# Optimization experiments

Measured on AMD Instinct MI355X. Metric: run time of the kernel, lower is better.

## Reference

```python
import jax, jax.numpy as jnp
import numpy as np

EMBED_DIM = 1024
NUM_HEADS = 16
HEAD_DIM = EMBED_DIM // NUM_HEADS
SCALE = float(np.sqrt(HEAD_DIM))


def setup_inputs() -> dict:
    key = jax.random.key(0)
    ks = jax.random.split(key, 7)
    B, S, E = 2, 2048, EMBED_DIM
    query = jax.random.normal(ks[0], (B, S, E), dtype=jnp.float32)
    key_t = jax.random.normal(ks[1], (B, S, E), dtype=jnp.float32)
    value = jax.random.normal(ks[2], (B, S, E), dtype=jnp.float32)
    # nn.Linear(E, E, bias=False): weight shape (out, in); y = x @ W.T
    std = 1.0 / np.sqrt(E)
    Wq = jax.random.uniform(ks[3], (E, E), jnp.float32, -std, std)
    Wk = jax.random.uniform(ks[4], (E, E), jnp.float32, -std, std)
    Wv = jax.random.uniform(ks[5], (E, E), jnp.float32, -std, std)
    Wo = jax.random.uniform(ks[6], (E, E), jnp.float32, -std, std)
    return {"query": query, "key": key_t, "value": value,
            "Wq": Wq, "Wk": Wk, "Wv": Wv, "Wo": Wo}


def reference(query, key, value, Wq, Wk, Wv, Wo):
    B, S, E = query.shape
    H, D = NUM_HEADS, HEAD_DIM
    q = (query @ Wq.T).reshape(B, S, H, D).transpose(0, 2, 1, 3)  # [B,H,S,D]
    k = (key @ Wk.T).reshape(B, S, H, D).transpose(0, 2, 1, 3)
    v = (value @ Wv.T).reshape(B, S, H, D).transpose(0, 2, 1, 3)
    scores = jnp.einsum('bhqd,bhkd->bhqk', q, k) / SCALE  # [B,H,S,S]
    attn = jax.nn.softmax(scores, axis=-1)
    out = jnp.einsum('bhqk,bhkd->bhqd', attn, v)  # [B,H,S,D]
    out = out.transpose(0, 2, 1, 3).reshape(B, S, E)
    return out @ Wo.T
```

## Files before the change

### kernel.cpp

```cpp
#include <hip/hip_runtime.h>
#include <hip/hip_bf16.h>
#include <math.h>

typedef float f32x4 __attribute__((ext_vector_type(4)));
typedef __bf16 bf16x8 __attribute__((ext_vector_type(8)));
typedef unsigned short u16;
typedef u16 u16x8 __attribute__((ext_vector_type(8)));
typedef u16 u16x4 __attribute__((ext_vector_type(4)));

__device__ __forceinline__ u16 f2bf(float f) {
    unsigned u = __builtin_bit_cast(unsigned, f);
    u = (u + 0x7fffu + ((u >> 16) & 1u)) >> 16;
    return (u16)u;
}
__device__ __forceinline__ unsigned pack2_rhu(float a, float b) {
    return __builtin_amdgcn_perm(__builtin_bit_cast(unsigned, b) + 0x8000u,
                                 __builtin_bit_cast(unsigned, a) + 0x8000u,
                                 0x07060302u);
}

#if __has_builtin(__builtin_amdgcn_exp2f)
#define EXP2(x) __builtin_amdgcn_exp2f(x)
#else
#define EXP2(x) exp2f(x)
#endif

__device__ __forceinline__ void gload16(const u16* g, u16* l) {
    __builtin_amdgcn_global_load_lds(
        (const __attribute__((address_space(1))) unsigned int*)(g),
        (__attribute__((address_space(3))) unsigned int*)(l), 16, 0, 0);
}

__global__ __launch_bounds__(256) void cast_all(
    const float* __restrict__ q, const float* __restrict__ k, const float* __restrict__ v,
    const float* __restrict__ wq, const float* __restrict__ wk, const float* __restrict__ wv,
    const float* __restrict__ wo, u16* __restrict__ dst) {
    int i = blockIdx.x * 256 + threadIdx.x;
    const float* src;
    int off;
    if (i < 3145728) {
        int seg = i >> 20;
        src = (seg == 0) ? q : (seg == 1) ? k : v;
        off = i - (seg << 20);
    } else {
        int j = (i - 3145728) >> 18;
        src = (j == 0) ? wq : (j == 1) ? wk : (j == 2) ? wv : wo;
        off = (i - 3145728) - (j << 18);
    }
    float4 val = ((const float4*)src)[off];
    u16x4 o4;
    o4.x = f2bf(val.x); o4.y = f2bf(val.y); o4.z = f2bf(val.z); o4.w = f2bf(val.w);
    ((u16x4*)dst)[i] = o4;
}

__global__ __launch_bounds__(256) void qkv_gemm(
    const u16* __restrict__ Xq, const u16* __restrict__ Xk, const u16* __restrict__ Xv,
    const u16* __restrict__ Wq, const u16* __restrict__ Wk, const u16* __restrict__ Wv,
    u16* __restrict__ Qo, u16* __restrict__ Ko, u16* __restrict__ Vto) {
    constexpr int K = 1024;
    const int z = blockIdx.z;
    const u16* __restrict__ A = (z == 0) ? Xq : (z == 1) ? Xk : Xv;
    const u16* __restrict__ W = (z == 0) ? Wq : (z == 1) ? Wk : Wv;
    u16* __restrict__ Out = (z == 0) ? Qo : (z == 1) ? Ko : Vto;

    __shared__ __align__(16) u16 As[128 * 64];
    __shared__ __align__(16) u16 Bs[128 * 64];

    const int t = threadIdx.x;
    const int lane = t & 63, wave = t >> 6;
    const int quad = lane >> 4, c = lane & 15, cx = c & 7;
    const int wr = (wave >> 1) * 64, wc = (wave & 1) * 64;
    const int rowA0 = blockIdx.y * 128;
    const int colB0 = blockIdx.x * 128;

    const int l3 = lane >> 3, l7 = lane & 7;
    const int chs = (l7 ^ l3) << 3;
    const u16* gA[4];
    const u16* gB[4];
    u16* lA[4];
    u16* lB[4];
#pragma unroll
    for (int i = 0; i < 4; ++i) {
        int row = wave * 32 + i * 8 + l3;
        gA[i] = A + (size_t)(rowA0 + row) * K + chs;
        gB[i] = W + (size_t)(colB0 + row) * K + chs;
        lA[i] = As + (wave * 256 + i * 64) * 8;
        lB[i] = Bs + (wave * 256 + i * 64) * 8;
    }

    const f32x4 zero4 = {0.f, 0.f, 0.f, 0.f};
    f32x4 acc[4][4];
#pragma unroll
    for (int i = 0; i < 4; ++i)
#pragma unroll
        for (int j = 0; j < 4; ++j) acc[i][j] = zero4;

    for (int kt = 0; kt < K; kt += 64) {
        __syncthreads();
#pragma unroll
        for (int i = 0; i < 4; ++i) {
            gload16(gA[i] + kt, lA[i]);
            gload16(gB[i] + kt, lB[i]);
        }
        __syncthreads();
#pragma unroll
        for (int ks = 0; ks < 2; ++ks) {
            const int co = ((ks * 4 + quad) ^ cx) << 3;
            bf16x8 af[4], bfr[4];
#pragma unroll
            for (int i = 0; i < 4; ++i)
                af[i] = *(const bf16x8*)(As + (wr + i * 16 + c) * 64 + co);
#pragma unroll
            for (int j = 0; j < 4; ++j)
                bfr[j] = *(const bf16x8*)(Bs + (wc + j * 16 + c) * 64 + co);
            if (z == 2) {
#pragma unroll
                for (int i = 0; i < 4; ++i)
#pragma unroll
                    for (int j = 0; j < 4; ++j)
                        acc[i][j] = __builtin_amdgcn_mfma_f32_16x16x32_bf16(bfr[j], af[i], acc[i][j], 0, 0, 0);
            } else {
#pragma unroll
                for (int i = 0; i < 4; ++i)
#pragma unroll
                    for (int j = 0; j < 4; ++j)
                        acc[i][j] = __builtin_amdgcn_mfma_f32_16x16x32_bf16(af[i], bfr[j], acc[i][j], 0, 0, 0);
            }
        }
    }

    const float scale = (z == 0) ? 0.18033688011112042f : 1.0f;
#pragma unroll
    for (int i = 0; i < 4; ++i) {
#pragma unroll
        for (int j = 0; j < 4; ++j) {
#pragma unroll
            for (int r = 0; r < 4; ++r) {
                float v = acc[i][j][r];
                if (z == 2) {
                    int n = colB0 + wc + j * 16 + quad * 4 + r;
                    int m = rowA0 + wr + i * 16 + c;
                    int b = m >> 11, s = m & 2047, h = n >> 6, d = n & 63;
                    Out[((((b << 4) | h) << 6) + d) * 2048 + s] = f2bf(v);
                } else {
                    int m = rowA0 + wr + i * 16 + quad * 4 + r;
                    int n = colB0 + wc + j * 16 + c;
                    int b = m >> 11, s = m & 2047, h = n >> 6, d = n & 63;
                    Out[((((b << 4) | h) * 2048 + s) << 6) + d] = f2bf(v * scale);
                }
            }
        }
    }
}

__global__ __launch_bounds__(256, 2) void out_gemm(const u16* __restrict__ A,
                                                   const u16* __restrict__ W,
                                                   float* __restrict__ Out) {
    constexpr int K = 1024;
    __shared__ __align__(16) u16 As[64 * 64];
    __shared__ __align__(16) u16 Bs[128 * 64];
    const int t = threadIdx.x;
    const int lane = t & 63, wave = t >> 6;
    const int quad = lane >> 4, c = lane & 15, cx = c & 7;
    const int wr = (wave >> 1) * 32, wc = (wave & 1) * 64;
    const int rowA0 = blockIdx.y * 64;
    const int colB0 = blockIdx.x * 128;

    const int l3 = lane >> 3, l7 = lane & 7;
    const int chs = (l7 ^ l3) << 3;
    const u16* gA[2];
    const u16* gB[4];
    u16* lA[2];
    u16* lB[4];
#pragma unroll
    for (int i = 0; i < 2; ++i) {
        int row = wave * 16 + i * 8 + l3;
        gA[i] = A + (size_t)(rowA0 + row) * K + chs;
        lA[i] = As + (wave * 128 + i * 64) * 8;
    }
#pragma unroll
    for (int i = 0; i < 4; ++i) {
        int row = wave * 32 + i * 8 + l3;
        gB[i] = W + (size_t)(colB0 + row) * K + chs;
        lB[i] = Bs + (wave * 256 + i * 64) * 8;
    }

    const f32x4 zero4 = {0.f, 0.f, 0.f, 0.f};
    f32x4 acc[2][4];
#pragma unroll
    for (int i = 0; i < 2; ++i)
#pragma unroll
        for (int j = 0; j < 4; ++j) acc[i][j] = zero4;

    for (int kt = 0; kt < K; kt += 64) {
        __syncthreads();
#pragma unroll
        for (int i = 0; i < 2; ++i) gload16(gA[i] + kt, lA[i]);
#pragma unroll
        for (int i = 0; i < 4; ++i) gload16(gB[i] + kt, lB[i]);
        __syncthreads();
#pragma unroll
        for (int ks = 0; ks < 2; ++ks) {
            const int co = ((ks * 4 + quad) ^ cx) << 3;
            bf16x8 af[2], bfr[4];
#pragma unroll
            for (int i = 0; i < 2; ++i)
                af[i] = *(const bf16x8*)(As + (wr + i * 16 + c) * 64 + co);
#pragma unroll
            for (int j = 0; j < 4; ++j)
                bfr[j] = *(const bf16x8*)(Bs + (wc + j * 16 + c) * 64 + co);
#pragma unroll
            for (int i = 0; i < 2; ++i)
#pragma unroll
                for (int j = 0; j < 4; ++j)
                    acc[i][j] = __builtin_amdgcn_mfma_f32_16x16x32_bf16(af[i], bfr[j], acc[i][j], 0, 0, 0);
        }
    }
#pragma unroll
    for (int i = 0; i < 2; ++i)
#pragma unroll
        for (int j = 0; j < 4; ++j)
#pragma unroll
            for (int r = 0; r < 4; ++r) {
                int m = rowA0 + wr + i * 16 + quad * 4 + r;
                int n = colB0 + wc + j * 16 + c;
                Out[(m << 10) + n] = acc[i][j][r];
            }
}

__global__ __launch_bounds__(256, 2) void flash_attn(const u16* __restrict__ Qp,
                                                     const u16* __restrict__ Kp,
                                                     const u16* __restrict__ Vt,
                                                     u16* __restrict__ Ob) {
    constexpr int S = 2048;
    const int bh = blockIdx.y;
    const int b = bh >> 4, h = bh & 15;
    const int t = threadIdx.x, wave = t >> 6, lane = t & 63;
    const int quad = lane >> 4, c = lane & 15, cx = c & 7;
    const int qw = blockIdx.x * 128 + wave * 32;
    const u16* Qb = Qp + (bh * S + qw) * 64;
    const u16* Kb = Kp + (bh * S) * 64;
    const u16* Vb = Vt + bh * 64 * S;

    __shared__ __align__(16) u16 Ks[2][64 * 64];
    __shared__ __align__(16) u16 Vs[2][64 * 64];
    __shared__ __align__(16) u16 Ps[4][32 * 64];
    u16* Pw = &Ps[wave][0];

    bf16x8 qf[2][2];
#pragma unroll
    for (int qt = 0; qt < 2; ++qt)
#pragma unroll
        for (int hf = 0; hf < 2; ++hf)
            qf[qt][hf] = *(const bf16x8*)(Qb + (qt * 16 + c) * 64 + hf * 32 + quad * 8);

    const int l3 = lane >> 3, l7 = lane & 7;
    const int chs = (l7 ^ l3) << 3;
    const u16* gK[2];
    const u16* gV[2];
    int lbase[2];
#pragma unroll
    for (int i = 0; i < 2; ++i) {
        int row = wave * 16 + i * 8 + l3;
        gK[i] = Kb + row * 64 + chs;
        gV[i] = Vb + row * 2048 + chs;
        lbase[i] = (wave * 128 + i * 64) * 8;
    }
#pragma unroll
    for (int i = 0; i < 2; ++i) {
        gload16(gK[i], &Ks[0][lbase[i]]);
        gload16(gV[i], &Vs[0][lbase[i]]);
    }
    __syncthreads();

    const f32x4 zero4 = {0.f, 0.f, 0.f, 0.f};
    f32x4 o[2][4];
#pragma unroll
    for (int qt = 0; qt < 2; ++qt)
#pragma unroll
        for (int t2 = 0; t2 < 4; ++t2) o[qt][t2] = zero4;
    float lsum[2] = {0.f, 0.f};

    for (int it = 0; it < S / 64; ++it) {
        const int cur = it & 1;
        if (it + 1 < S / 64) {
#pragma unroll
            for (int i = 0; i < 2; ++i) {
                gload16(gK[i] + (it + 1) * 4096, &Ks[cur ^ 1][lbase[i]]);
                gload16(gV[i] + (it + 1) * 64, &Vs[cur ^ 1][lbase[i]]);
            }
        }
        const u16* Kc = &Ks[cur][0];
        const u16* Vc = &Vs[cur][0];
        const int co0 = (quad ^ cx) << 3, co1 = ((4 + quad) ^ cx) << 3;
        f32x4 sc[4][2];
#pragma unroll
        for (int kt = 0; kt < 4; ++kt) {
            const int krow = (kt * 16 + c) * 64;
            bf16x8 kf0 = *(const bf16x8*)(Kc + krow + co0);
            bf16x8 kf1 = *(const bf16x8*)(Kc + krow + co1);
#pragma unroll
            for (int qt = 0; qt < 2; ++qt) {
                f32x4 zz = zero4;
                zz = __builtin_amdgcn_mfma_f32_16x16x32_bf16(kf0, qf[qt][0], zz, 0, 0, 0);
                zz = __builtin_amdgcn_mfma_f32_16x16x32_bf16(kf1, qf[qt][1], zz, 0, 0, 0);
                sc[kt][qt] = zz;
            }
        }
#pragma unroll
        for (int kt = 0; kt < 4; ++kt) {
            const int pchunk = ((kt * 2 + (quad >> 1)) ^ cx) << 3;
#pragma unroll
            for (int qt = 0; qt < 2; ++qt) {
                float p0 = EXP2(sc[kt][qt][0]);
                float p1 = EXP2(sc[kt][qt][1]);
                float p2 = EXP2(sc[kt][qt][2]);
                float p3 = EXP2(sc[kt][qt][3]);
                lsum[qt] += (p0 + p1) + (p2 + p3);
                uint2 pk;
                pk.x = pack2_rhu(p0, p1);
                pk.y = pack2_rhu(p2, p3);
                *(uint2*)(Pw + (qt * 16 + c) * 64 + pchunk + (quad & 1) * 4) = pk;
            }
        }
        __asm__ __volatile__("s_waitcnt lgkmcnt(0)" ::: "memory");
        bf16x8 pf[2][2];
#pragma unroll
        for (int qt = 0; qt < 2; ++qt) {
            pf[qt][0] = *(const bf16x8*)(Pw + (qt * 16 + c) * 64 + co0);
            pf[qt][1] = *(const bf16x8*)(Pw + (qt * 16 + c) * 64 + co1);
        }
#pragma unroll
        for (int t2 = 0; t2 < 4; ++t2) {
            const int vrow = (t2 * 16 + c) * 64;
            bf16x8 vf0 = *(const bf16x8*)(Vc + vrow + co0);
            bf16x8 vf1 = *(const bf16x8*)(Vc + vrow + co1);
#pragma unroll
            for (int qt = 0; qt < 2; ++qt) {
                o[qt][t2] = __builtin_amdgcn_mfma_f32_16x16x32_bf16(pf[qt][0], vf0, o[qt][t2], 0, 0, 0);
                o[qt][t2] = __builtin_amdgcn_mfma_f32_16x16x32_bf16(pf[qt][1], vf1, o[qt][t2], 0, 0, 0);
            }
        }
        __syncthreads();
    }
#pragma unroll
    for (int qt = 0; qt < 2; ++qt) {
        lsum[qt] += __shfl_xor(lsum[qt], 16);
        lsum[qt] += __shfl_xor(lsum[qt], 32);
    }
#pragma unroll
    for (int qt = 0; qt < 2; ++qt)
#pragma unroll
        for (int r = 0; r < 4; ++r) {
            float inv = 1.f / __shfl(lsum[qt], quad * 4 + r);
            int row = qw + qt * 16 + quad * 4 + r;
            int base = ((b * S + row) * 16 + h) * 64;
#pragma unroll
            for (int t2 = 0; t2 < 4; ++t2)
                Ob[base + t2 * 16 + c] = f2bf(o[qt][t2][r] * inv);
        }
}

extern "C" void kernel_launch(void* const* d_in, const int* in_sizes, int n_in,
                              void* d_out, int out_size, void* d_ws, size_t ws_size,
                              hipStream_t stream) {
    const float* q  = (const float*)d_in[0];
    const float* k  = (const float*)d_in[1];
    const float* v  = (const float*)d_in[2];
    const float* wq = (const float*)d_in[3];
    const float* wk = (const float*)d_in[4];
    const float* wv = (const float*)d_in[5];
    const float* wo = (const float*)d_in[6];

    u16* ws = (u16*)d_ws;
    u16* qb  = ws;
    u16* kb  = ws + 4194304;
    u16* vb  = ws + 8388608;
    u16* wqb = ws + 12582912;
    u16* wkb = ws + 13631488;
    u16* wvb = ws + 14680064;
    u16* wob = ws + 15728640;
    u16* Qp  = ws + 16777216;
    u16* Kp  = ws + 20971520;
    u16* Vtp = ws + 25165824;
    u16* Obf = ws + 29360128;

    cast_all<<<16384, 256, 0, stream>>>(q, k, v, wq, wk, wv, wo, ws);

    qkv_gemm<<<dim3(8, 32, 3), 256, 0, stream>>>(qb, kb, vb, wqb, wkb, wvb, Qp, Kp, Vtp);

    flash_attn<<<dim3(16, 32), 256, 0, stream>>>(Qp, Kp, Vtp, Obf);

    out_gemm<<<dim3(8, 64), 256, 0, stream>>>(Obf, wob, (float*)d_out);
}
```

Before: 221.5 us.

## Software-pipeline attention loop: overlap previous P·V with current QK^T

Restructures the flash-attention main loop so the P·V MFMAs for tile it-1 run after the QK^T MFMAs for tile it and before the exp/pack of tile it. This breaks the serial dependency between softmax and the P·V product. It adds a third V buffer, double-buffers the per-wave P tile, and moves the final P·V into an epilogue. It also drops the occupancy hint from launch_bounds, and the larger shared memory use may lower occupancy.

```diff
diff --git a/kernel.cpp b/kernel.cpp
--- a/kernel.cpp
+++ b/kernel.cpp
@@ -228,11 +228,12 @@
             }
 }
 
-__global__ __launch_bounds__(256, 2) void flash_attn(const u16* __restrict__ Qp,
-                                                     const u16* __restrict__ Kp,
-                                                     const u16* __restrict__ Vt,
-                                                     u16* __restrict__ Ob) {
+__global__ __launch_bounds__(256) void flash_attn(const u16* __restrict__ Qp,
+                                                  const u16* __restrict__ Kp,
+                                                  const u16* __restrict__ Vt,
+                                                  u16* __restrict__ Ob) {
     constexpr int S = 2048;
+    constexpr int NT = S / 64;
     const int bh = blockIdx.y;
     const int b = bh >> 4, h = bh & 15;
     const int t = threadIdx.x, wave = t >> 6, lane = t & 63;
@@ -243,9 +244,8 @@
     const u16* Vb = Vt + bh * 64 * S;
 
     __shared__ __align__(16) u16 Ks[2][64 * 64];
-    __shared__ __align__(16) u16 Vs[2][64 * 64];
-    __shared__ __align__(16) u16 Ps[4][32 * 64];
-    u16* Pw = &Ps[wave][0];
+    __shared__ __align__(16) u16 Vs[3][64 * 64];
+    __shared__ __align__(16) u16 Ps[4][2][32 * 64];
 
     bf16x8 qf[2][2];
 #pragma unroll
@@ -281,18 +281,18 @@
         for (int t2 = 0; t2 < 4; ++t2) o[qt][t2] = zero4;
     float lsum[2] = {0.f, 0.f};
 
-    for (int it = 0; it < S / 64; ++it) {
-        const int cur = it & 1;
-        if (it + 1 < S / 64) {
+    const int co0 = (quad ^ cx) << 3, co1 = ((4 + quad) ^ cx) << 3;
+    int vb_prev = 2, vb_cur = 0, vb_next = 1;
+
+    for (int it = 0; it < NT; ++it) {
+        if (it + 1 < NT) {
 #pragma unroll
             for (int i = 0; i < 2; ++i) {
-                gload16(gK[i] + (it + 1) * 4096, &Ks[cur ^ 1][lbase[i]]);
-                gload16(gV[i] + (it + 1) * 64, &Vs[cur ^ 1][lbase[i]]);
-            }
-        }
-        const u16* Kc = &Ks[cur][0];
-        const u16* Vc = &Vs[cur][0];
-        const int co0 = (quad ^ cx) << 3, co1 = ((4 + quad) ^ cx) << 3;
+                gload16(gK[i] + (it + 1) * 4096, &Ks[(it + 1) & 1][lbase[i]]);
+                gload16(gV[i] + (it + 1) * 64, &Vs[vb_next][lbase[i]]);
+            }
+        }
+        const u16* Kc = &Ks[it & 1][0];
         f32x4 sc[4][2];
 #pragma unroll
         for (int kt = 0; kt < 4; ++kt) {
@@ -307,6 +307,28 @@
                 sc[kt][qt] = zz;
             }
         }
+        if (it > 0) {
+            const u16* Pwp = &Ps[wave][(it - 1) & 1][0];
+            const u16* Vc = &Vs[vb_prev][0];
+            bf16x8 pf[2][2];
+#pragma unroll
+            for (int qt = 0; qt < 2; ++qt) {
+                pf[qt][0] = *(const bf16x8*)(Pwp + (qt * 16 + c) * 64 + co0);
+                pf[qt][1] = *(const bf16x8*)(Pwp + (qt * 16 + c) * 64 + co1);
+            }
+#pragma unroll
+            for (int t2 = 0; t2 < 4; ++t2) {
+                const int vrow = (t2 * 16 + c) * 64;
+                bf16x8 vf0 = *(const bf16x8*)(Vc + vrow + co0);
+                bf16x8 vf1 = *(const bf16x8*)(Vc + vrow + co1);
+#pragma unroll
+                for (int qt = 0; qt < 2; ++qt) {
+                    o[qt][t2] = __builtin_amdgcn_mfma_f32_16x16x32_bf16(pf[qt][0], vf0, o[qt][t2], 0, 0, 0);
+                    o[qt][t2] = __builtin_amdgcn_mfma_f32_16x16x32_bf16(pf[qt][1], vf1, o[qt][t2], 0, 0, 0);
+                }
+            }
+        }
+        u16* Pwc = &Ps[wave][it & 1][0];
 #pragma unroll
         for (int kt = 0; kt < 4; ++kt) {
             const int pchunk = ((kt * 2 + (quad >> 1)) ^ cx) << 3;
@@ -320,15 +342,23 @@
                 uint2 pk;
                 pk.x = pack2_rhu(p0, p1);
                 pk.y = pack2_rhu(p2, p3);
-                *(uint2*)(Pw + (qt * 16 + c) * 64 + pchunk + (quad & 1) * 4) = pk;
-            }
-        }
-        __asm__ __volatile__("s_waitcnt lgkmcnt(0)" ::: "memory");
+                *(uint2*)(Pwc + (qt * 16 + c) * 64 + pchunk + (quad & 1) * 4) = pk;
+            }
+        }
+        __syncthreads();
+        int tmp = vb_prev;
+        vb_prev = vb_cur;
+        vb_cur = vb_next;
+        vb_next = tmp;
+    }
+    {
+        const u16* Pwp = &Ps[wave][(NT - 1) & 1][0];
+        const u16* Vc = &Vs[vb_prev][0];
         bf16x8 pf[2][2];
 #pragma unroll
         for (int qt = 0; qt < 2; ++qt) {
-            pf[qt][0] = *(const bf16x8*)(Pw + (qt * 16 + c) * 64 + co0);
-            pf[qt][1] = *(const bf16x8*)(Pw + (qt * 16 + c) * 64 + co1);
+            pf[qt][0] = *(const bf16x8*)(Pwp + (qt * 16 + c) * 64 + co0);
+            pf[qt][1] = *(const bf16x8*)(Pwp + (qt * 16 + c) * 64 + co1);
         }
 #pragma unroll
         for (int t2 = 0; t2 < 4; ++t2) {
@@ -341,7 +371,6 @@
                 o[qt][t2] = __builtin_amdgcn_mfma_f32_16x16x32_bf16(pf[qt][1], vf1, o[qt][t2], 0, 0, 0);
             }
         }
-        __syncthreads();
     }
 #pragma unroll
     for (int qt = 0; qt < 2; ++qt) {
```

Measured after the change: 227.9 us. +2.9%, slower.
